# Performance work log

Measured on AMD Instinct MI355X. Metric: run time of the kernel, lower is better.

## Reference

```python
import jax, jax.numpy as jnp
import numpy as np

K_PERIODS = 4
PMAX = 64
MIN_PERIOD = 8


def setup_inputs() -> dict:
    key = jax.random.key(0)
    x = jax.random.normal(key, (32, 512, 64), dtype=jnp.float32)  # [B, T, N]
    return {"x": x}


def reference(x):
    """Dense, fixed-shape equivalent of PeriodicityTransform.forward (mask=None).

    Instead of a Python list of variable-shape PeriodGroup tiles, returns a
    padded tensor values[bn, k, c, p] where for each (sequence bn, freq rank k)
    with period P and cycles C, values[bn, k, :C, :P] equals the torch tile
    seqs[bn, T-C*P : T].reshape(C, P); entries outside (C, P) are zero.
    Also returns the integer periods and cycles per (bn, k).
    """
    B, T, N = x.shape
    BN = B * N
    seqs = jnp.transpose(x, (0, 2, 1)).reshape(BN, T)  # [BN, T]

    # top-k nonzero FFT frequencies (DC bin zeroed out)
    spec = jnp.fft.rfft(seqs, axis=-1)
    mag2 = spec.real ** 2 + spec.imag ** 2
    mag2 = mag2.at[..., 0].set(0.0)
    _, kidx = jax.lax.top_k(mag2, K_PERIODS)  # [BN, K]
    kidx = jnp.maximum(kidx, 1)

    # periods = clamp(T // f, min=MIN_PERIOD, max=PMAX); cycles = T // period
    periods = jnp.clip(T // kidx, MIN_PERIOD, PMAX)  # [BN, K]
    cycles = T // periods                              # [BN, K]

    cmax = T // MIN_PERIOD  # static upper bound on cycles
    i = jnp.arange(cmax)[:, None]   # cycle index  [Cmax, 1]
    j = jnp.arange(PMAX)[None, :]   # phase index  [1, Pmax]

    start = T - cycles * periods                                   # [BN, K]
    idx = start[..., None, None] + i * periods[..., None, None] + j  # [BN,K,Cmax,Pmax]
    idx = jnp.clip(idx, 0, T - 1)
    valid = (i < cycles[..., None, None]) & (j < periods[..., None, None])

    gathered = jnp.take_along_axis(
        seqs[:, None, :], idx.reshape(BN, K_PERIODS, -1), axis=-1
    ).reshape(BN, K_PERIODS, cmax, PMAX)
    values = jnp.where(valid, gathered, jnp.float32(0.0))
    return values, periods, cycles
```

## Files before the change

kernel.cpp:

```cpp
#include <hip/hip_runtime.h>
#include <math.h>

#define TT 512
#define KP 4

typedef unsigned long long u64;

#define SYNCL() asm volatile("s_waitcnt lgkmcnt(0)\n\ts_barrier" ::: "memory")

__global__ __launch_bounds__(256) void periodicity_kernel(const float* __restrict__ x,
                                                          float* __restrict__ out) {
    const int bn   = blockIdx.x;
    const int tid  = threadIdx.x;
    const int lane = tid & 63;
    const int wid  = tid >> 6;
    const int b = bn >> 6;
    const int n = bn & 63;

    __shared__ float2 tw[TT];
    __shared__ __align__(16) float row[TT];
    __shared__ float2 buf[TT];
    __shared__ u64    keys[256];
    __shared__ int    fin8[8];
    __shared__ float  candMagF[8];
    __shared__ double candV8[8];

    float sv, cv;
    sincosf((float)(2.0 * M_PI / 512.0) * (float)tid, &sv, &cv);
    tw[tid]       = make_float2(cv, -sv);
    tw[tid + 256] = make_float2(-cv, sv);

    const float* xb = x + (size_t)b * (TT * 64) + n;
    {
        float v0 = xb[(size_t)tid * 64];
        float v1 = xb[(size_t)(tid + 256) * 64];
        row[tid] = v0;  row[tid + 256] = v1;
        float sum = v0 + v1, dif = v0 - v1;
        buf[tid]       = make_float2(sum, 0.f);
        buf[tid + 256] = make_float2(dif * cv, -dif * sv);
    }
    SYNCL();

    #pragma unroll
    for (int stg = 0; stg < 3; ++stg) {
        if (tid < 128) {
            const int Q  = 64 >> (2 * stg);
            const int B4 = Q << 2;
            const int h  = tid >> 6;
            const int fj = tid & 63;
            const int g  = fj >> (6 - 2 * stg);
            const int i  = fj & (Q - 1);
            float2* bb = &buf[h << 8];
            const int base = g * B4 + i;
            float2 x0 = bb[base],         x1 = bb[base + Q];
            float2 x2 = bb[base + 2 * Q], x3 = bb[base + 3 * Q];
            float2 A  = make_float2(x0.x + x2.x, x0.y + x2.y);
            float2 Bm = make_float2(x0.x - x2.x, x0.y - x2.y);
            float2 Cc = make_float2(x1.x + x3.x, x1.y + x3.y);
            float2 D  = make_float2(x1.x - x3.x, x1.y - x3.y);
            float2 y0 = make_float2(A.x + Cc.x, A.y + Cc.y);
            float2 y2 = make_float2(A.x - Cc.x, A.y - Cc.y);
            float2 y1 = make_float2(Bm.x + D.y, Bm.y - D.x);
            float2 y3 = make_float2(Bm.x - D.y, Bm.y + D.x);
            const int m = i << (1 + 2 * stg);
            float2 t1 = tw[m], t2 = tw[2 * m], t3 = tw[3 * m];
            bb[base]         = y0;
            bb[base + Q]     = make_float2(y1.x * t1.x - y1.y * t1.y, y1.x * t1.y + y1.y * t1.x);
            bb[base + 2 * Q] = make_float2(y2.x * t2.x - y2.y * t2.y, y2.x * t2.y + y2.y * t2.x);
            bb[base + 3 * Q] = make_float2(y3.x * t3.x - y3.y * t3.y, y3.x * t3.y + y3.y * t3.x);
        }
        SYNCL();
    }

    if (tid < 128) {
        const int h = tid >> 6;
        const int g = tid & 63;
        float2* bb = &buf[h << 8];
        const int base = g << 2;
        float2 x0 = bb[base],     x1 = bb[base + 1];
        float2 x2 = bb[base + 2], x3 = bb[base + 3];
        float2 A  = make_float2(x0.x + x2.x, x0.y + x2.y);
        float2 Bm = make_float2(x0.x - x2.x, x0.y - x2.y);
        float2 Cc = make_float2(x1.x + x3.x, x1.y + x3.y);
        float2 D  = make_float2(x1.x - x3.x, x1.y - x3.y);
        float2 y0 = make_float2(A.x + Cc.x, A.y + Cc.y);
        float2 y2 = make_float2(A.x - Cc.x, A.y - Cc.y);
        float2 y1 = make_float2(Bm.x + D.y, Bm.y - D.x);
        float2 y3 = make_float2(Bm.x - D.y, Bm.y + D.x);
        const int revg = ((g & 3) << 4) | (((g >> 2) & 3) << 2) | ((g >> 4) & 3);
        const int f0 = 2 * revg + h;
        float mags[4];
        mags[0] = y0.x * y0.x + y0.y * y0.y;
        mags[1] = y1.x * y1.x + y1.y * y1.y;
        mags[2] = y2.x * y2.x + y2.y * y2.y;
        mags[3] = y3.x * y3.x + y3.y * y3.y;
        #pragma unroll
        for (int j = 0; j < 4; ++j) {
            const int f = f0 + 128 * j;
            if (f >= 1 && f <= 256)
                keys[f - 1] = ((u64)__float_as_uint(mags[j]) << 32) | (u64)(255 - (f - 1));
        }
    }
    SYNCL();

    if (wid == 0) {
        u64 k0 = keys[lane * 4 + 0];
        u64 k1 = keys[lane * 4 + 1];
        u64 k2 = keys[lane * 4 + 2];
        u64 k3 = keys[lane * 4 + 3];
        #define CSWAP(a, b) { if (a < b) { u64 _t = a; a = b; b = _t; } }
        CSWAP(k0, k1) CSWAP(k2, k3) CSWAP(k0, k2) CSWAP(k1, k3) CSWAP(k1, k2)
        #undef CSWAP
        #pragma unroll
        for (int r = 0; r < 8; ++r) {
            u64 w = k0;
            #pragma unroll
            for (int off = 32; off >= 1; off >>= 1) {
                u64 o = __shfl_xor(w, off);
                if (o > w) w = o;
            }
            if (k0 == w) { k0 = k1; k1 = k2; k2 = k3; k3 = 0; }
            if (lane == 0) {
                fin8[r] = 256 - (int)(w & 0xff);
                candMagF[r] = __uint_as_float((unsigned)(w >> 32));
            }
        }
    }
    SYNCL();

    int per[KP], cycv[KP], stv[KP];
    {
        const float m0 = candMagF[0], m1 = candMagF[1], m2 = candMagF[2],
                    m3 = candMagF[3], m4 = candMagF[4];
        const bool needRefine = ((m0 - m1) <= 1e-4f * m0) || ((m1 - m2) <= 1e-4f * m1) ||
                                ((m2 - m3) <= 1e-4f * m2) || ((m3 - m4) <= 1e-4f * m3);
        int bins[KP];
        if (!needRefine) {
            #pragma unroll
            for (int k = 0; k < KP; ++k) bins[k] = fin8[k];
        } else {
            {
                const int cid = tid >> 5;
                const int sub = tid & 31;
                const int fc  = fin8[cid];
                const int t0  = sub * 16;
                const double W = 6.2831853071795864769 / 512.0;
                double zr, zi, wr, wi;
                sincos(W * (double)((fc * t0) & 511), &zi, &zr);
                sincos(W * (double)fc, &wi, &wr);
                double ar = 0.0, ai = 0.0;
                const float4* r4 = (const float4*)row;
                #pragma unroll
                for (int v4i = 0; v4i < 4; ++v4i) {
                    float4 xv = r4[sub * 4 + v4i];
                    #define STEP(comp)                                   \
                        { double xd = (double)xv.comp;                   \
                          ar = fma(xd, zr, ar); ai = fma(xd, zi, ai);    \
                          double tq = zr * wr - zi * wi;                 \
                          zi = fma(zr, wi, zi * wr); zr = tq; }
                    STEP(x) STEP(y) STEP(z) STEP(w)
                    #undef STEP
                }
                #pragma unroll
                for (int off = 16; off >= 1; off >>= 1) {
                    ar += __shfl_xor(ar, off);
                    ai += __shfl_xor(ai, off);
                }
                if (sub == 0) candV8[cid] = ar * ar + ai * ai;
            }
            SYNCL();
            unsigned chosen = 0;
            #pragma unroll
            for (int k = 0; k < KP; ++k) {
                double bv = -1.0; int bbin = 0x7fffffff; int bj = 0;
                #pragma unroll
                for (int j = 0; j < 8; ++j) {
                    if (chosen & (1u << j)) continue;
                    double vj = candV8[j];
                    int    bjn = fin8[j];
                    if (vj > bv || (vj == bv && bjn < bbin)) { bv = vj; bbin = bjn; bj = j; }
                }
                chosen |= (1u << bj);
                bins[k] = bbin;
            }
        }
        #pragma unroll
        for (int k = 0; k < KP; ++k) {
            int p = TT / bins[k];
            p = p < 8 ? 8 : (p > 64 ? 64 : p);
            per[k]  = p;
            cycv[k] = TT / p;
            stv[k]  = TT - cycv[k] * p;
        }
    }

    const size_t VOFF = (size_t)2048 * KP * 64 * 64;
    if (tid == 0) {
        #pragma unroll
        for (int k = 0; k < KP; ++k) {
            out[VOFF + (size_t)bn * KP + k]        = (float)per[k];
            out[VOFF + 8192 + (size_t)bn * KP + k] = (float)cycv[k];
        }
    }

    float* outv = out + (size_t)bn * (KP * 64 * 64);
    const int c_local = tid >> 4;
    const int p0 = (tid & 15) << 2;
    #pragma unroll
    for (int it = 0; it < 16; ++it) {
        const int k = it >> 2;
        const int c = ((it & 3) << 4) + c_local;
        float4 v = make_float4(0.f, 0.f, 0.f, 0.f);
        const int P = per[k], C = cycv[k], S0 = stv[k];
        if (c < C) {
            const int base = S0 + c * P;
            if (p0 + 3 < P) {
                v.x = row[base + p0];
                v.y = row[base + p0 + 1];
                v.z = row[base + p0 + 2];
                v.w = row[base + p0 + 3];
            } else {
                if (p0     < P) v.x = row[base + p0];
                if (p0 + 1 < P) v.y = row[base + p0 + 1];
                if (p0 + 2 < P) v.z = row[base + p0 + 2];
                if (p0 + 3 < P) v.w = row[base + p0 + 3];
            }
        }
        *(float4*)(outv + (size_t)it * 1024 + (size_t)tid * 4) = v;
    }
}

extern "C" void kernel_launch(void* const* d_in, const int* in_sizes, int n_in,
                              void* d_out, int out_size, void* d_ws, size_t ws_size,
                              hipStream_t stream) {
    const float* x = (const float*)d_in[0];
    float* out = (float*)d_out;
    hipLaunchKernelGGL(periodicity_kernel, dim3(2048), dim3(256), 0, stream, x, out);
}
```

Before: 30.47 us.

## Replace block barriers in FFT with wave-local sync and redundant per-wave top-k

Each of the two FFT halves is now handled by a single wavefront, so the per-stage block barriers become wave-local lgkmcnt waits. Every wave runs the top-k shuffle reduction redundantly in registers, which removes the shared fin8/candMagF arrays and one block barrier. Keys are written and read as 128-bit vector accesses, and the block index is remapped so that neighbouring blocks read different batch slices. The extra redundant work in the other waves and the switch-based register indexing add some instructions and register pressure.

```diff
diff --git a/kernel.cpp b/kernel.cpp
--- a/kernel.cpp
+++ b/kernel.cpp
@@ -7,10 +7,12 @@
 typedef unsigned long long u64;
 
 #define SYNCL() asm volatile("s_waitcnt lgkmcnt(0)\n\ts_barrier" ::: "memory")
+#define SYNCW() do { asm volatile("s_waitcnt lgkmcnt(0)" ::: "memory"); \
+                     __builtin_amdgcn_sched_barrier(0); } while (0)
 
 __global__ __launch_bounds__(256) void periodicity_kernel(const float* __restrict__ x,
                                                           float* __restrict__ out) {
-    const int bn   = blockIdx.x;
+    const int bn   = (blockIdx.x & 7) * 256 + (blockIdx.x >> 3);
     const int tid  = threadIdx.x;
     const int lane = tid & 63;
     const int wid  = tid >> 6;
@@ -19,10 +21,8 @@
 
     __shared__ float2 tw[TT];
     __shared__ __align__(16) float row[TT];
-    __shared__ float2 buf[TT];
-    __shared__ u64    keys[256];
-    __shared__ int    fin8[8];
-    __shared__ float  candMagF[8];
+    __shared__ __align__(16) float2 buf[TT];
+    __shared__ __align__(16) u64 keys[256];
     __shared__ double candV8[8];
 
     float sv, cv;
@@ -41,17 +41,16 @@
     }
     SYNCL();
 
-    #pragma unroll
-    for (int stg = 0; stg < 3; ++stg) {
-        if (tid < 128) {
+    if (wid < 2) {
+        const int h = wid;
+        float2* bb = &buf[h << 8];
+
+        #pragma unroll
+        for (int stg = 0; stg < 3; ++stg) {
             const int Q  = 64 >> (2 * stg);
-            const int B4 = Q << 2;
-            const int h  = tid >> 6;
-            const int fj = tid & 63;
-            const int g  = fj >> (6 - 2 * stg);
-            const int i  = fj & (Q - 1);
-            float2* bb = &buf[h << 8];
-            const int base = g * B4 + i;
+            const int g  = lane >> (6 - 2 * stg);
+            const int i  = lane & (Q - 1);
+            const int base = g * (Q << 2) + i;
             float2 x0 = bb[base],         x1 = bb[base + Q];
             float2 x2 = bb[base + 2 * Q], x3 = bb[base + 3 * Q];
             float2 A  = make_float2(x0.x + x2.x, x0.y + x2.y);
@@ -68,46 +67,49 @@
             bb[base + Q]     = make_float2(y1.x * t1.x - y1.y * t1.y, y1.x * t1.y + y1.y * t1.x);
             bb[base + 2 * Q] = make_float2(y2.x * t2.x - y2.y * t2.y, y2.x * t2.y + y2.y * t2.x);
             bb[base + 3 * Q] = make_float2(y3.x * t3.x - y3.y * t3.y, y3.x * t3.y + y3.y * t3.x);
-        }
-        SYNCL();
-    }
-
-    if (tid < 128) {
-        const int h = tid >> 6;
-        const int g = tid & 63;
-        float2* bb = &buf[h << 8];
-        const int base = g << 2;
-        float2 x0 = bb[base],     x1 = bb[base + 1];
-        float2 x2 = bb[base + 2], x3 = bb[base + 3];
-        float2 A  = make_float2(x0.x + x2.x, x0.y + x2.y);
-        float2 Bm = make_float2(x0.x - x2.x, x0.y - x2.y);
-        float2 Cc = make_float2(x1.x + x3.x, x1.y + x3.y);
-        float2 D  = make_float2(x1.x - x3.x, x1.y - x3.y);
-        float2 y0 = make_float2(A.x + Cc.x, A.y + Cc.y);
-        float2 y2 = make_float2(A.x - Cc.x, A.y - Cc.y);
-        float2 y1 = make_float2(Bm.x + D.y, Bm.y - D.x);
-        float2 y3 = make_float2(Bm.x - D.y, Bm.y + D.x);
-        const int revg = ((g & 3) << 4) | (((g >> 2) & 3) << 2) | ((g >> 4) & 3);
-        const int f0 = 2 * revg + h;
-        float mags[4];
-        mags[0] = y0.x * y0.x + y0.y * y0.y;
-        mags[1] = y1.x * y1.x + y1.y * y1.y;
-        mags[2] = y2.x * y2.x + y2.y * y2.y;
-        mags[3] = y3.x * y3.x + y3.y * y3.y;
-        #pragma unroll
-        for (int j = 0; j < 4; ++j) {
-            const int f = f0 + 128 * j;
-            if (f >= 1 && f <= 256)
-                keys[f - 1] = ((u64)__float_as_uint(mags[j]) << 32) | (u64)(255 - (f - 1));
+            SYNCW();
+        }
+
+        {
+            const int g = lane;
+            const int base = g << 2;
+            float2 x0 = bb[base],     x1 = bb[base + 1];
+            float2 x2 = bb[base + 2], x3 = bb[base + 3];
+            float2 A  = make_float2(x0.x + x2.x, x0.y + x2.y);
+            float2 Bm = make_float2(x0.x - x2.x, x0.y - x2.y);
+            float2 Cc = make_float2(x1.x + x3.x, x1.y + x3.y);
+            float2 D  = make_float2(x1.x - x3.x, x1.y - x3.y);
+            float2 y0 = make_float2(A.x + Cc.x, A.y + Cc.y);
+            float2 y2 = make_float2(A.x - Cc.x, A.y - Cc.y);
+            float2 y1 = make_float2(Bm.x + D.y, Bm.y - D.x);
+            float2 y3 = make_float2(Bm.x - D.y, Bm.y + D.x);
+            const int revg = ((g & 3) << 4) | (((g >> 2) & 3) << 2) | ((g >> 4) & 3);
+            const int f0 = 2 * revg + h;
+            float m0 = y0.x * y0.x + y0.y * y0.y;
+            float m1 = y1.x * y1.x + y1.y * y1.y;
+            float m2 = y2.x * y2.x + y2.y * y2.y;
+            float m3 = y3.x * y3.x + y3.y * y3.y;
+            u64 kA, kB;
+            if (f0 == 0) {
+                kA = ((u64)__float_as_uint(m1) << 32) | (u64)(256 - 128);
+                kB = ((u64)__float_as_uint(m2) << 32) | (u64)(256 - 256);
+            } else {
+                kA = ((u64)__float_as_uint(m0) << 32) | (u64)(256 - f0);
+                kB = ((u64)__float_as_uint(m1) << 32) | (u64)(256 - (f0 + 128));
+            }
+            ulonglong2* kv = (ulonglong2*)keys;
+            kv[(h << 6) + g] = make_ulonglong2(kA, kB);
         }
     }
     SYNCL();
 
-    if (wid == 0) {
-        u64 k0 = keys[lane * 4 + 0];
-        u64 k1 = keys[lane * 4 + 1];
-        u64 k2 = keys[lane * 4 + 2];
-        u64 k3 = keys[lane * 4 + 3];
+    int   fbin[8];
+    float cmag[8];
+    {
+        const ulonglong2* kv = (const ulonglong2*)keys;
+        ulonglong2 p0v = kv[lane * 2];
+        ulonglong2 p1v = kv[lane * 2 + 1];
+        u64 k0 = p0v.x, k1 = p0v.y, k2 = p1v.x, k3 = p1v.y;
         #define CSWAP(a, b) { if (a < b) { u64 _t = a; a = b; b = _t; } }
         CSWAP(k0, k1) CSWAP(k2, k3) CSWAP(k0, k2) CSWAP(k1, k3) CSWAP(k1, k2)
         #undef CSWAP
@@ -120,30 +122,36 @@
                 if (o > w) w = o;
             }
             if (k0 == w) { k0 = k1; k1 = k2; k2 = k3; k3 = 0; }
-            if (lane == 0) {
-                fin8[r] = 256 - (int)(w & 0xff);
-                candMagF[r] = __uint_as_float((unsigned)(w >> 32));
-            }
-        }
-    }
-    SYNCL();
+            fbin[r] = 256 - (int)(w & 0xff);
+            cmag[r] = __uint_as_float((unsigned)(w >> 32));
+        }
+    }
 
     int per[KP], cycv[KP], stv[KP];
     {
-        const float m0 = candMagF[0], m1 = candMagF[1], m2 = candMagF[2],
-                    m3 = candMagF[3], m4 = candMagF[4];
-        const bool needRefine = ((m0 - m1) <= 1e-4f * m0) || ((m1 - m2) <= 1e-4f * m1) ||
-                                ((m2 - m3) <= 1e-4f * m2) || ((m3 - m4) <= 1e-4f * m3);
+        const bool needRefine =
+            ((cmag[0] - cmag[1]) <= 1e-4f * cmag[0]) || ((cmag[1] - cmag[2]) <= 1e-4f * cmag[1]) ||
+            ((cmag[2] - cmag[3]) <= 1e-4f * cmag[2]) || ((cmag[3] - cmag[4]) <= 1e-4f * cmag[3]);
         int bins[KP];
         if (!needRefine) {
             #pragma unroll
-            for (int k = 0; k < KP; ++k) bins[k] = fin8[k];
+            for (int k = 0; k < KP; ++k) bins[k] = fbin[k];
         } else {
             {
                 const int cid = tid >> 5;
                 const int sub = tid & 31;
-                const int fc  = fin8[cid];
-                const int t0  = sub * 16;
+                int fc;
+                switch (cid) {
+                    case 0: fc = fbin[0]; break;
+                    case 1: fc = fbin[1]; break;
+                    case 2: fc = fbin[2]; break;
+                    case 3: fc = fbin[3]; break;
+                    case 4: fc = fbin[4]; break;
+                    case 5: fc = fbin[5]; break;
+                    case 6: fc = fbin[6]; break;
+                    default: fc = fbin[7]; break;
+                }
+                const int t0 = sub * 16;
                 const double W = 6.2831853071795864769 / 512.0;
                 double zr, zi, wr, wi;
                 sincos(W * (double)((fc * t0) & 511), &zi, &zr);
@@ -177,7 +185,7 @@
                 for (int j = 0; j < 8; ++j) {
                     if (chosen & (1u << j)) continue;
                     double vj = candV8[j];
-                    int    bjn = fin8[j];
+                    int    bjn = fbin[j];
                     if (vj > bv || (vj == bv && bjn < bbin)) { bv = vj; bbin = bjn; bj = j; }
                 }
                 chosen |= (1u << bj);
```

Measured after the change: 30.48 us. About the same (+0.0%).
